# Optimization experiments

Hardware: AMD Instinct MI355X
Metric: run time of the kernel (lower is better)

## Reference

```python
import jax, jax.numpy as jnp
import numpy as np

N, K, N_OF, N_EF, H = 16384, 32, 7, 1, 1


def setup_inputs() -> dict:
    key = jax.random.key(0)
    ks = jax.random.split(key, 8)
    return {
        "object_features": jax.random.normal(ks[0], (N, K, N_OF), dtype=jnp.float32),
        "edge_features": jax.random.uniform(ks[1], (N, K, K, N_EF), dtype=jnp.float32),
        "action": jax.random.normal(ks[2], (N, N_OF), dtype=jnp.float32),
        "W_ni": jax.random.normal(ks[3], (2 * N_OF, H), dtype=jnp.float32) / np.sqrt(2 * N_OF),
        "b_ni": jnp.zeros((H,), dtype=jnp.float32),
        "W_e": jax.random.normal(ks[4], (2 * H + N_EF, H), dtype=jnp.float32) / np.sqrt(2 * H + N_EF),
        "b_e": jnp.zeros((H,), dtype=jnp.float32),
        "W_n": jax.random.normal(ks[5], (H, H), dtype=jnp.float32),
        "b_n": jnp.zeros((H,), dtype=jnp.float32),
        "W_ef": jax.random.normal(ks[6], (H, N_EF), dtype=jnp.float32),
        "b_ef": jnp.zeros((N_EF,), dtype=jnp.float32),
    }


def reference(object_features, edge_features, action, W_ni, b_ni, W_e, b_e, W_n, b_n, W_ef, b_ef):
    n, k, _ = object_features.shape
    # embed: concat node features with broadcast action, Linear (no activation)
    a = jnp.broadcast_to(action[:, None, :], object_features.shape)  # (N,K,n_of)
    xa = jnp.concatenate([object_features, a], axis=-1)              # (N,K,2*n_of)
    hn = xa @ W_ni + b_ni                                            # (N,K,H)

    def edge_fn(hn):
        x = jnp.broadcast_to(hn[:, :, None, :], (n, k, k, hn.shape[-1]))  # sender
        xxe = jnp.concatenate([x, jnp.swapaxes(x, 1, 2), edge_features], axis=-1)
        return jax.nn.relu(xxe @ W_e + b_e)                          # (N,K,K,H)

    # one message-passing round (I = 1)
    he = edge_fn(hn)
    hn = jax.nn.relu(he.sum(axis=2) @ W_n + b_n)                     # (N,K,H)
    # final edge update + edge readout
    he = edge_fn(hn)
    hef = jax.nn.relu(he @ W_ef + b_ef)                              # (N,K,K,n_ef)
    return jax.nn.sigmoid(hef)  # pred_type == 'full_state'
```

## Files before the change

kernel.cpp:

```cpp
#include <hip/hip_runtime.h>
#include <math.h>


#define KK 32

__global__ __launch_bounds__(256) void gnn_fused_kernel(
    const float* __restrict__ of,
    const float* __restrict__ ef,
    const float* __restrict__ act,
    const float* __restrict__ W_ni,
    const float* __restrict__ b_ni,
    const float* __restrict__ W_e,
    const float* __restrict__ b_e,
    const float* __restrict__ W_n,
    const float* __restrict__ b_n,
    const float* __restrict__ W_ef,
    const float* __restrict__ b_ef,
    float* __restrict__ out)
{
    const int n = blockIdx.x;
    const int t = threadIdx.x;

    __shared__ float s_hn[KK];
    __shared__ float s_row[KK];
    __shared__ float s_hn2[KK];

    const float we0 = W_e[0], we1 = W_e[1], we2 = W_e[2], be = b_e[0];
    const float wn  = W_n[0],  bn  = b_n[0];
    const float wef = W_ef[0], bef = b_ef[0];

    if (t < KK) {
        const float* ofp = of + ((size_t)n * KK + t) * 7;
        const float* ap  = act + (size_t)n * 7;
        float s = b_ni[0];
        #pragma unroll
        for (int f = 0; f < 7; ++f) s += ofp[f] * W_ni[f];
        #pragma unroll
        for (int f = 0; f < 7; ++f) s += ap[f] * W_ni[7 + f];
        s_hn[t] = s;
    }
    __syncthreads();

    const int i  = t >> 3;
    const int j0 = (t & 7) * 4;
    const float4 e4 = *reinterpret_cast<const float4*>(
        ef + ((size_t)n * KK + i) * KK + j0);

    const float hni = s_hn[i];
    const float hj0 = s_hn[j0 + 0], hj1 = s_hn[j0 + 1];
    const float hj2 = s_hn[j0 + 2], hj3 = s_hn[j0 + 3];

    float part =
        fmaxf(fmaf(we2, e4.x, fmaf(we1, hj0, fmaf(we0, hni, be))), 0.f) +
        fmaxf(fmaf(we2, e4.y, fmaf(we1, hj1, fmaf(we0, hni, be))), 0.f) +
        fmaxf(fmaf(we2, e4.z, fmaf(we1, hj2, fmaf(we0, hni, be))), 0.f) +
        fmaxf(fmaf(we2, e4.w, fmaf(we1, hj3, fmaf(we0, hni, be))), 0.f);

    part += __shfl_xor(part, 1);
    part += __shfl_xor(part, 2);
    part += __shfl_xor(part, 4);
    if ((t & 7) == 0) s_row[i] = part;
    __syncthreads();

    if (t < KK) s_hn2[t] = fmaxf(fmaf(wn, s_row[t], bn), 0.f);
    __syncthreads();

    const float g_i  = s_hn2[i];
    const float g_j0 = s_hn2[j0 + 0], g_j1 = s_hn2[j0 + 1];
    const float g_j2 = s_hn2[j0 + 2], g_j3 = s_hn2[j0 + 3];

    float4 o4;
    {
        float v = fmaxf(fmaf(we2, e4.x, fmaf(we1, g_j0, fmaf(we0, g_i, be))), 0.f);
        v = fmaxf(fmaf(wef, v, bef), 0.f);
        o4.x = 1.f / (1.f + expf(-v));
    }
    {
        float v = fmaxf(fmaf(we2, e4.y, fmaf(we1, g_j1, fmaf(we0, g_i, be))), 0.f);
        v = fmaxf(fmaf(wef, v, bef), 0.f);
        o4.y = 1.f / (1.f + expf(-v));
    }
    {
        float v = fmaxf(fmaf(we2, e4.z, fmaf(we1, g_j2, fmaf(we0, g_i, be))), 0.f);
        v = fmaxf(fmaf(wef, v, bef), 0.f);
        o4.z = 1.f / (1.f + expf(-v));
    }
    {
        float v = fmaxf(fmaf(we2, e4.w, fmaf(we1, g_j3, fmaf(we0, g_i, be))), 0.f);
        v = fmaxf(fmaf(wef, v, bef), 0.f);
        o4.w = 1.f / (1.f + expf(-v));
    }

    *reinterpret_cast<float4*>(out + ((size_t)n * KK + i) * KK + j0) = o4;
}

extern "C" void kernel_launch(void* const* d_in, const int* in_sizes, int n_in,
                              void* d_out, int out_size, void* d_ws, size_t ws_size,
                              hipStream_t stream) {
    const float* of   = (const float*)d_in[0];
    const float* ef   = (const float*)d_in[1];
    const float* act  = (const float*)d_in[2];
    const float* W_ni = (const float*)d_in[3];
    const float* b_ni = (const float*)d_in[4];
    const float* W_e  = (const float*)d_in[5];
    const float* b_e  = (const float*)d_in[6];
    const float* W_n  = (const float*)d_in[7];
    const float* b_n  = (const float*)d_in[8];
    const float* W_ef = (const float*)d_in[9];
    const float* b_ef = (const float*)d_in[10];
    float* out = (float*)d_out;

    const int N = in_sizes[2] / 7;
    gnn_fused_kernel<<<N, 256, 0, stream>>>(
        of, ef, act, W_ni, b_ni, W_e, b_e, W_n, b_n, W_ef, b_ef, out);
}
```

Before: 30.46 us.

## Map one graph per wavefront with shuffle-based exchange instead of shared memory

Each 64-lane wavefront now processes a whole graph (4 graphs per 256-thread block), holding all 1024 edge features in registers as four float4 per lane. Node embeddings and row sums are exchanged with wave shuffles instead of LDS and __syncthreads. It also issues all edge loads up front, uses the fast __expf intrinsic, and writes the output with nontemporal stores. This removes block-wide barriers and LDS traffic and cuts the block count by four, at the cost of more registers per thread and a small loss of precision in the exponential.

After: 28.27 us. 7.2% less time.

```diff
diff --git a/kernel.cpp b/kernel.cpp
--- a/kernel.cpp
+++ b/kernel.cpp
@@ -2,7 +2,7 @@
 #include <math.h>
 
 
-#define KK 32
+typedef float v4f __attribute__((ext_vector_type(4)));
 
 __global__ __launch_bounds__(256) void gnn_fused_kernel(
     const float* __restrict__ of,
@@ -16,82 +16,88 @@
     const float* __restrict__ b_n,
     const float* __restrict__ W_ef,
     const float* __restrict__ b_ef,
-    float* __restrict__ out)
+    float* __restrict__ out,
+    int Ntot)
 {
-    const int n = blockIdx.x;
-    const int t = threadIdx.x;
+    const int wv = threadIdx.x >> 6;
+    const int l  = threadIdx.x & 63;
+    const int n  = blockIdx.x * 4 + wv;
+    if (n >= Ntot) return;
 
-    __shared__ float s_hn[KK];
-    __shared__ float s_row[KK];
-    __shared__ float s_hn2[KK];
+    const float* efp = ef + (size_t)n * 1024;
+    float4 e[4];
+    #pragma unroll
+    for (int q = 0; q < 4; ++q)
+        e[q] = *reinterpret_cast<const float4*>(efp + q * 256 + l * 4);
 
     const float we0 = W_e[0], we1 = W_e[1], we2 = W_e[2], be = b_e[0];
     const float wn  = W_n[0],  bn  = b_n[0];
     const float wef = W_ef[0], bef = b_ef[0];
 
-    if (t < KK) {
-        const float* ofp = of + ((size_t)n * KK + t) * 7;
+    float hn_own = 0.f;
+    if (l < 32) {
+        const float* ofp = of + ((size_t)n * 32 + l) * 7;
         const float* ap  = act + (size_t)n * 7;
         float s = b_ni[0];
         #pragma unroll
-        for (int f = 0; f < 7; ++f) s += ofp[f] * W_ni[f];
+        for (int f = 0; f < 7; ++f) s = fmaf(ofp[f], W_ni[f], s);
         #pragma unroll
-        for (int f = 0; f < 7; ++f) s += ap[f] * W_ni[7 + f];
-        s_hn[t] = s;
-    }
-    __syncthreads();
-
-    const int i  = t >> 3;
-    const int j0 = (t & 7) * 4;
-    const float4 e4 = *reinterpret_cast<const float4*>(
-        ef + ((size_t)n * KK + i) * KK + j0);
-
-    const float hni = s_hn[i];
-    const float hj0 = s_hn[j0 + 0], hj1 = s_hn[j0 + 1];
-    const float hj2 = s_hn[j0 + 2], hj3 = s_hn[j0 + 3];
-
-    float part =
-        fmaxf(fmaf(we2, e4.x, fmaf(we1, hj0, fmaf(we0, hni, be))), 0.f) +
-        fmaxf(fmaf(we2, e4.y, fmaf(we1, hj1, fmaf(we0, hni, be))), 0.f) +
-        fmaxf(fmaf(we2, e4.z, fmaf(we1, hj2, fmaf(we0, hni, be))), 0.f) +
-        fmaxf(fmaf(we2, e4.w, fmaf(we1, hj3, fmaf(we0, hni, be))), 0.f);
-
-    part += __shfl_xor(part, 1);
-    part += __shfl_xor(part, 2);
-    part += __shfl_xor(part, 4);
-    if ((t & 7) == 0) s_row[i] = part;
-    __syncthreads();
-
-    if (t < KK) s_hn2[t] = fmaxf(fmaf(wn, s_row[t], bn), 0.f);
-    __syncthreads();
-
-    const float g_i  = s_hn2[i];
-    const float g_j0 = s_hn2[j0 + 0], g_j1 = s_hn2[j0 + 1];
-    const float g_j2 = s_hn2[j0 + 2], g_j3 = s_hn2[j0 + 3];
-
-    float4 o4;
-    {
-        float v = fmaxf(fmaf(we2, e4.x, fmaf(we1, g_j0, fmaf(we0, g_i, be))), 0.f);
-        v = fmaxf(fmaf(wef, v, bef), 0.f);
-        o4.x = 1.f / (1.f + expf(-v));
-    }
-    {
-        float v = fmaxf(fmaf(we2, e4.y, fmaf(we1, g_j1, fmaf(we0, g_i, be))), 0.f);
-        v = fmaxf(fmaf(wef, v, bef), 0.f);
-        o4.y = 1.f / (1.f + expf(-v));
-    }
-    {
-        float v = fmaxf(fmaf(we2, e4.z, fmaf(we1, g_j2, fmaf(we0, g_i, be))), 0.f);
-        v = fmaxf(fmaf(wef, v, bef), 0.f);
-        o4.z = 1.f / (1.f + expf(-v));
-    }
-    {
-        float v = fmaxf(fmaf(we2, e4.w, fmaf(we1, g_j3, fmaf(we0, g_i, be))), 0.f);
-        v = fmaxf(fmaf(wef, v, bef), 0.f);
-        o4.w = 1.f / (1.f + expf(-v));
+        for (int f = 0; f < 7; ++f) s = fmaf(ap[f], W_ni[7 + f], s);
+        hn_own = s;
     }
 
-    *reinterpret_cast<float4*>(out + ((size_t)n * KK + i) * KK + j0) = o4;
+    const int m     = l >> 3;
+    const int jbase = (l & 7) * 4;
+
+    float hn_j[4];
+    #pragma unroll
+    for (int k = 0; k < 4; ++k) hn_j[k] = __shfl(hn_own, jbase + k);
+
+    float s_q[4];
+    #pragma unroll
+    for (int q = 0; q < 4; ++q) {
+        const float hni = __shfl(hn_own, q * 8 + m);
+        const float a   = fmaf(we0, hni, be);
+        const float* ec = reinterpret_cast<const float*>(&e[q]);
+        float p = 0.f;
+        #pragma unroll
+        for (int k = 0; k < 4; ++k)
+            p += fmaxf(fmaf(we2, ec[k], fmaf(we1, hn_j[k], a)), 0.f);
+        p += __shfl_xor(p, 1);
+        p += __shfl_xor(p, 2);
+        p += __shfl_xor(p, 4);
+        s_q[q] = p;
+    }
+
+    float a0 = __shfl(s_q[0], (l & 7) * 8);
+    float a1 = __shfl(s_q[1], (l & 7) * 8);
+    float a2 = __shfl(s_q[2], (l & 7) * 8);
+    float a3 = __shfl(s_q[3], (l & 7) * 8);
+    float b0 = (l & 8)  ? a1 : a0;
+    float b1 = (l & 8)  ? a3 : a2;
+    float sum_own = (l & 16) ? b1 : b0;
+
+    const float hn2_own = fmaxf(fmaf(wn, sum_own, bn), 0.f);
+
+    float g_j[4];
+    #pragma unroll
+    for (int k = 0; k < 4; ++k) g_j[k] = __shfl(hn2_own, jbase + k);
+
+    float* outp = out + (size_t)n * 1024;
+    #pragma unroll
+    for (int q = 0; q < 4; ++q) {
+        const float g_i = __shfl(hn2_own, q * 8 + m);
+        const float a   = fmaf(we0, g_i, be);
+        const float* ec = reinterpret_cast<const float*>(&e[q]);
+        v4f o;
+        #pragma unroll
+        for (int k = 0; k < 4; ++k) {
+            float v = fmaxf(fmaf(we2, ec[k], fmaf(we1, g_j[k], a)), 0.f);
+            v = fmaxf(fmaf(wef, v, bef), 0.f);
+            o[k] = 1.f / (1.f + __expf(-v));
+        }
+        __builtin_nontemporal_store(o, (v4f*)(outp + q * 256 + l * 4));
+    }
 }
 
 extern "C" void kernel_launch(void* const* d_in, const int* in_sizes, int n_in,
@@ -111,6 +117,7 @@
     float* out = (float*)d_out;
 
     const int N = in_sizes[2] / 7;
-    gnn_fused_kernel<<<N, 256, 0, stream>>>(
-        of, ef, act, W_ni, b_ni, W_e, b_e, W_n, b_n, W_ef, b_ef, out);
+    const int blocks = (N + 3) / 4;
+    gnn_fused_kernel<<<blocks, 256, 0, stream>>>(
+        of, ef, act, W_ni, b_ni, W_e, b_e, W_n, b_n, W_ef, b_ef, out, N);
 }
```
